# Kernel tuning notes

Measured on AMD Instinct MI355X. Metric: run time of the kernel, lower is better.

## Reference

```python
import jax, jax.numpy as jnp
import numpy as np

L = 6   # n_layers
NH = 8  # num_heads


def _ln(x, g, b, eps=1e-5):
    m = jnp.mean(x, axis=-1, keepdims=True)
    v = jnp.var(x, axis=-1, keepdims=True)
    return (x - m) / jnp.sqrt(v + eps) * g + b


def _mha(q_in, k_in, v_in, Wqkv, bqkv, Wo, bo, bias):
    # Wqkv: [3,H,H], bias: [B,NH,Sq,Sk] or None
    B, Sq, H = q_in.shape
    dk = H // NH
    q = (q_in @ Wqkv[0] + bqkv[0]).reshape(B, Sq, NH, dk).transpose(0, 2, 1, 3)
    k = (k_in @ Wqkv[1] + bqkv[1]).reshape(B, -1, NH, dk).transpose(0, 2, 1, 3)
    v = (v_in @ Wqkv[2] + bqkv[2]).reshape(B, -1, NH, dk).transpose(0, 2, 1, 3)
    scores = jnp.einsum('bhqd,bhkd->bhqk', q * (dk ** -0.5), k)
    if bias is not None:
        scores = scores + bias
    a = jax.nn.softmax(scores, axis=-1)
    o = jnp.einsum('bhqk,bhkd->bhqd', a, v).transpose(0, 2, 1, 3).reshape(B, Sq, H)
    return o @ Wo + bo


def setup_inputs() -> dict:
    key = jax.random.key(0)
    B, N, Din, H, Bd, F, C, G, Dout = 8, 512, 128, 512, 8, 2048, 128, 1, 10
    ks = jax.random.split(key, 20)
    s = 0.02 / np.sqrt(L)
    inp = {
        'x': jax.random.normal(ks[0], (B, N, Din), jnp.float32),
        'attn_bias': jax.random.normal(ks[1], (B, N, N, Bd), jnp.float32),
        'node_W': jax.random.normal(ks[2], (Din, H), jnp.float32) * s,
        'node_b': jnp.zeros((H,), jnp.float32),
        'graph_token': jax.random.normal(ks[3], (G, H), jnp.float32) * 0.02,
        'graph_vd': jax.random.normal(ks[4], (G, Bd), jnp.float32) * 0.02,
        'centroids': jax.random.uniform(ks[5], (C, H), jnp.float32),
        'ln1_g': jnp.ones((L, H), jnp.float32),
        'ln1_b': jnp.zeros((L, H), jnp.float32),
        'Wqkv_loc': jax.random.normal(ks[6], (L, 3, H, H), jnp.float32) * s,
        'bqkv_loc': jnp.zeros((L, 3, H), jnp.float32),
        'Wbias': jax.random.normal(ks[7], (L, Bd, NH), jnp.float32) * s,
        'bbias': jnp.zeros((L, NH), jnp.float32),
        'Wo_loc': jax.random.normal(ks[8], (L, H, H), jnp.float32) * s,
        'bo_loc': jnp.zeros((L, H), jnp.float32),
        'Wqkv_glb': jax.random.normal(ks[9], (L, 3, H, H), jnp.float32) * s,
        'bqkv_glb': jnp.zeros((L, 3, H), jnp.float32),
        'Wo_glb': jax.random.normal(ks[10], (L, H, H), jnp.float32) * s,
        'bo_glb': jnp.zeros((L, H), jnp.float32),
        'ffn_ln_g': jnp.ones((L, 2 * H), jnp.float32),
        'ffn_ln_b': jnp.zeros((L, 2 * H), jnp.float32),
        'W1': jax.random.normal(ks[11], (L, 2 * H, F), jnp.float32) * s,
        'b1': jnp.zeros((L, F), jnp.float32),
        'W2': jax.random.normal(ks[12], (L, F, H), jnp.float32) * s,
        'b2': jnp.zeros((L, H), jnp.float32),
        'final_g': jnp.ones((H,), jnp.float32),
        'final_b': jnp.zeros((H,), jnp.float32),
        'out_W': jax.random.normal(ks[13], (H, Dout), jnp.float32) * s,
        'out_b': jnp.zeros((Dout,), jnp.float32),
    }
    return inp


def reference(x, attn_bias, node_W, node_b, graph_token, graph_vd, centroids,
              ln1_g, ln1_b, Wqkv_loc, bqkv_loc, Wbias, bbias, Wo_loc, bo_loc,
              Wqkv_glb, bqkv_glb, Wo_glb, bo_glb, ffn_ln_g, ffn_ln_b,
              W1, b1, W2, b2, final_g, final_b, out_W, out_b):
    B, N, _ = x.shape
    G = graph_token.shape[0]
    S = N + G
    # node encoder + global node tokens
    h = x @ node_W + node_b                                   # [B,N,H]
    h = jnp.concatenate([h, jnp.broadcast_to(graph_token[None], (B, G, graph_token.shape[1]))], axis=1)  # [B,S,H]
    # extend attn_bias with virtual-distance rows/cols -> [B,S,S,Bd]
    Bd = attn_bias.shape[-1]
    row = jnp.broadcast_to(graph_vd[None, :, None, :], (B, G, N, Bd))
    ab = jnp.concatenate([attn_bias, row], axis=1)            # [B,S,N,Bd]
    col = jnp.broadcast_to(graph_vd[None, None, :, :], (B, S, G, Bd))
    ab = jnp.concatenate([ab, col], axis=2)                   # [B,S,S,Bd]
    # centroids broadcast over batch
    c = jnp.broadcast_to(centroids[None], (B,) + centroids.shape)
    out = h
    for l in range(L):
        bias_l = jnp.einsum('bqkd,dh->bhqk', ab, Wbias[l]) + bbias[l][None, :, None, None]
        y = _ln(out, ln1_g[l], ln1_b[l])
        y = _mha(y, y, y, Wqkv_loc[l], bqkv_loc[l], Wo_loc[l], bo_loc[l], bias_l)
        xr = out + y
        g = _mha(y, c, c, Wqkv_glb[l], bqkv_glb[l], Wo_glb[l], bo_glb[l], None)
        g = xr + g
        y2 = _ln(jnp.concatenate([xr, g], axis=-1), ffn_ln_g[l], ffn_ln_b[l])
        y2 = jax.nn.gelu(y2 @ W1[l] + b1[l], approximate=False) @ W2[l] + b2[l]
        out = xr + y2
    out = _ln(out, final_g, final_b)
    logits = out[:, 0, :] @ out_W + out_b
    return jax.nn.log_softmax(logits, axis=1)
```

## Files before the change

kernel.cpp:

```cpp
#include <hip/hip_runtime.h>
#include <math.h>

typedef unsigned short ushort_t;
typedef __attribute__((ext_vector_type(8))) __bf16 bf16x8;
typedef __attribute__((ext_vector_type(4))) float f32x4;

#define BB 8
#define NN 512
#define HH 512
#define NH 8
#define DKK 64
#define FF 2048
#define CC 128
#define LL 6
#define SS 513
#define SQP 528
#define SPL 544
#define MV 4104
#define MP 4224

__device__ inline float b2f(ushort_t u){ unsigned int x = ((unsigned int)u) << 16; return __uint_as_float(x); }
__device__ inline ushort_t f2b(float f){
    unsigned int x = __float_as_uint(f);
    unsigned int r = (x + 0x7fffu + ((x >> 16) & 1u)) >> 16;
    return (ushort_t)r;
}

__global__ __launch_bounds__(256)
void transpose_cvt_k(const float* __restrict__ in, ushort_t* __restrict__ out, int K, int N){
    __shared__ float t[32][33];
    int z = blockIdx.z;
    in  += (size_t)z * K * N;
    out += (size_t)z * K * N;
    int n0 = blockIdx.x * 32, k0 = blockIdx.y * 32;
    int tx = threadIdx.x, ty = threadIdx.y;
    #pragma unroll
    for (int i = 0; i < 4; i++)
        t[ty + i*8][tx] = in[(size_t)(k0 + ty + i*8) * N + n0 + tx];
    __syncthreads();
    #pragma unroll
    for (int i = 0; i < 4; i++)
        out[(size_t)(n0 + ty + i*8) * K + k0 + tx] = f2b(t[tx][ty + i*8]);
}

__global__ __launch_bounds__(256)
void cvt_k(const float* __restrict__ in, ushort_t* __restrict__ out, int n4){
    int i = blockIdx.x * 256 + threadIdx.x;
    if (i < n4){
        float4 v = ((const float4*)in)[i];
        ushort4 o; o.x = f2b(v.x); o.y = f2b(v.y); o.z = f2b(v.z); o.w = f2b(v.w);
        ((ushort4*)out)[i] = o;
    }
}

__global__ void fill_graph_k(const float* __restrict__ gt, float* __restrict__ resid){
    int b = blockIdx.x, t = threadIdx.x;
    resid[((size_t)(b*SS) + NN)*HH + t] = gt[t];
}

struct EpiP {
    const float* bias;
    float* f0; const float* fin;
    ushort_t* b0; ushort_t* b1; ushort_t* b2;
    int Mvalid;
    int zsB, zsBias, zs0, zs1;
};

template<int EPI>
__global__ __launch_bounds__(256, 2)
void gemm_k(const ushort_t* __restrict__ Abuf, int lda,
            const ushort_t* __restrict__ Bt, int ldb,
            int K, EpiP p)
{
    __shared__ ushort_t As[2][128*64];
    __shared__ ushort_t Bs[2][128*64];
    int tid = threadIdx.x, lane = tid & 63, wave = tid >> 6;
    int z = blockIdx.z;
    Bt += (size_t)z * p.zsB;
    int tm = blockIdx.y * 128, tn = blockIdx.x * 128;
    int r0 = (wave >> 1) * 64, c0 = (wave & 1) * 64;
    int lrow = lane & 15, lk = (lane >> 4) * 8;
    const ushort_t* Ag0 = Abuf + (size_t)tm * lda;
    const ushort_t* Bg0 = Bt   + (size_t)tn * ldb;

    auto stage = [&](int buf, int k0){
        #pragma unroll
        for (int i = 0; i < 4; i++){
            int boff = (i*256 + tid) * 16;
            int row  = boff >> 7;
            int src  = boff ^ ((row & 7) << 4);
            int cole = (src & 127) >> 1;
            __builtin_amdgcn_global_load_lds(
                (const __attribute__((address_space(1))) void*)(Ag0 + (size_t)row*lda + k0 + cole),
                (__attribute__((address_space(3))) void*)((char*)As[buf] + boff), 16, 0, 0);
            __builtin_amdgcn_global_load_lds(
                (const __attribute__((address_space(1))) void*)(Bg0 + (size_t)row*ldb + k0 + cole),
                (__attribute__((address_space(3))) void*)((char*)Bs[buf] + boff), 16, 0, 0);
        }
    };

    f32x4 acc[4][4] = {};
    stage(0, 0);
    int nk = K >> 6;
    for (int kt = 0; kt < nk; kt++){
        int cur = kt & 1;
        __syncthreads();
        if (kt + 1 < nk) stage(cur ^ 1, (kt + 1) * 64);
        const char* Ac = (const char*)As[cur];
        const char* Bc = (const char*)Bs[cur];
        #pragma unroll
        for (int kk = 0; kk < 64; kk += 32){
            bf16x8 af[4], bfv[4];
            #pragma unroll
            for (int i = 0; i < 4; i++){
                int r = r0 + i*16 + lrow;
                int byte = (r*64 + kk + lk)*2;
                byte ^= (r & 7) << 4;
                af[i] = *(const bf16x8*)(Ac + byte);
            }
            #pragma unroll
            for (int j = 0; j < 4; j++){
                int r = c0 + j*16 + lrow;
                int byte = (r*64 + kk + lk)*2;
                byte ^= (r & 7) << 4;
                bfv[j] = *(const bf16x8*)(Bc + byte);
            }
            #pragma unroll
            for (int i = 0; i < 4; i++)
                #pragma unroll
                for (int j = 0; j < 4; j++)
                    acc[i][j] = __builtin_amdgcn_mfma_f32_16x16x32_bf16(af[i], bfv[j], acc[i][j], 0, 0, 0);
        }
    }
    const float* biasp = p.bias ? (p.bias + (size_t)z * p.zsBias) : nullptr;
    #pragma unroll
    for (int i = 0; i < 4; i++)
    #pragma unroll
    for (int j = 0; j < 4; j++)
    #pragma unroll
    for (int r = 0; r < 4; r++){
        int grow = tm + r0 + i*16 + (lane >> 4)*4 + r;
        int gcol = tn + c0 + j*16 + (lane & 15);
        if (grow >= p.Mvalid) continue;
        float v = acc[i][j][r] + (biasp ? biasp[gcol] : 0.f);
        if constexpr (EPI == 0){
            int rg = (grow >> 9) * SS + (grow & 511);
            p.f0[(size_t)rg * HH + gcol] = v;
        } else if constexpr (EPI == 1){
            int b = grow / SS, s = grow - b * SS;
            int mat = gcol >> 9, c = gcol & 511, h = c >> 6, d = c & 63;
            if (mat == 0)      p.b0[(((size_t)(b*NH + h))*SQP + s)*DKK + d] = f2b(v);
            else if (mat == 1) p.b1[(((size_t)(b*NH + h))*SPL + s)*DKK + d] = f2b(v);
            else               p.b2[(((size_t)(b*NH + h))*DKK + d)*SPL + s] = f2b(v);
        } else if constexpr (EPI == 2){
            int mat = gcol >> 9, c = gcol & 511, h = c >> 6, d = c & 63;
            if (mat == 0) (p.b0 + (size_t)z*p.zs0)[((size_t)h*CC + grow)*DKK + d] = f2b(v);
            else          (p.b1 + (size_t)z*p.zs1)[((size_t)h*DKK + d)*CC + grow] = f2b(v);
        } else if constexpr (EPI == 3){
            int b = grow / SS, s = grow - b * SS, h = gcol >> 6, d = gcol & 63;
            p.b0[(((size_t)(b*NH + h))*SQP + s)*DKK + d] = f2b(v);
        } else if constexpr (EPI == 4){
            p.b0[(size_t)grow*HH + gcol] = f2b(v);
            p.f0[(size_t)grow*HH + gcol] = p.fin[(size_t)grow*HH + gcol] + v;
        } else if constexpr (EPI == 5){
            p.f0[(size_t)grow*HH + gcol] = p.fin[(size_t)grow*HH + gcol] + v;
        } else if constexpr (EPI == 6){
            float t = 0.5f * v * (1.f + erff(v * 0.70710678118f));
            p.b0[(size_t)grow*FF + gcol] = f2b(t);
        } else if constexpr (EPI == 7){
            p.f0[(size_t)grow*HH + gcol] = p.fin[(size_t)grow*HH + gcol] + v;
        }
    }
}

__global__ __launch_bounds__(128)
void ln512_k(const float* __restrict__ in, const float* __restrict__ g,
             const float* __restrict__ bb, ushort_t* __restrict__ out){
    int row = blockIdx.x, t = threadIdx.x;
    float4 v = ((const float4*)(in + (size_t)row*HH))[t];
    float s  = v.x + v.y + v.z + v.w;
    float s2 = v.x*v.x + v.y*v.y + v.z*v.z + v.w*v.w;
    #pragma unroll
    for (int o = 1; o < 64; o <<= 1){ s += __shfl_xor(s, o); s2 += __shfl_xor(s2, o); }
    __shared__ float ps[2], ps2[2];
    if ((t & 63) == 0){ ps[t >> 6] = s; ps2[t >> 6] = s2; }
    __syncthreads();
    s = ps[0] + ps[1]; s2 = ps2[0] + ps2[1];
    float mean = s * (1.f/512.f);
    float var  = s2 * (1.f/512.f) - mean*mean;
    float rstd = rsqrtf(var + 1e-5f);
    float4 gv = ((const float4*)g)[t];
    float4 bv = ((const float4*)bb)[t];
    ushort4 o4;
    o4.x = f2b((v.x - mean)*rstd*gv.x + bv.x);
    o4.y = f2b((v.y - mean)*rstd*gv.y + bv.y);
    o4.z = f2b((v.z - mean)*rstd*gv.z + bv.z);
    o4.w = f2b((v.w - mean)*rstd*gv.w + bv.w);
    ((ushort4*)(out + (size_t)row*HH))[t] = o4;
}

__global__ __launch_bounds__(128)
void ln1024_k(const float* __restrict__ xr, const float* __restrict__ gb,
              const float* __restrict__ g, const float* __restrict__ bb,
              ushort_t* __restrict__ out){
    int row = blockIdx.x, t = threadIdx.x;
    const float* src = (t < 64) ? (xr + (size_t)row*HH + t*8) : (gb + (size_t)row*HH + (t-64)*8);
    float4 v0 = ((const float4*)src)[0];
    float4 v1 = ((const float4*)src)[1];
    float s  = v0.x+v0.y+v0.z+v0.w + v1.x+v1.y+v1.z+v1.w;
    float s2 = v0.x*v0.x+v0.y*v0.y+v0.z*v0.z+v0.w*v0.w + v1.x*v1.x+v1.y*v1.y+v1.z*v1.z+v1.w*v1.w;
    #pragma unroll
    for (int o = 1; o < 64; o <<= 1){ s += __shfl_xor(s, o); s2 += __shfl_xor(s2, o); }
    __shared__ float ps[2], ps2[2];
    if ((t & 63) == 0){ ps[t >> 6] = s; ps2[t >> 6] = s2; }
    __syncthreads();
    s = ps[0] + ps[1]; s2 = ps2[0] + ps2[1];
    float mean = s * (1.f/1024.f);
    float var  = s2 * (1.f/1024.f) - mean*mean;
    float rstd = rsqrtf(var + 1e-5f);
    int col = (t < 64) ? t*8 : 512 + (t-64)*8;
    float vv[8] = {v0.x,v0.y,v0.z,v0.w,v1.x,v1.y,v1.z,v1.w};
    ushort4 oa, ob;
    float r0 = (vv[0]-mean)*rstd*g[col+0] + bb[col+0];
    float r1 = (vv[1]-mean)*rstd*g[col+1] + bb[col+1];
    float r2 = (vv[2]-mean)*rstd*g[col+2] + bb[col+2];
    float r3 = (vv[3]-mean)*rstd*g[col+3] + bb[col+3];
    float r4 = (vv[4]-mean)*rstd*g[col+4] + bb[col+4];
    float r5 = (vv[5]-mean)*rstd*g[col+5] + bb[col+5];
    float r6 = (vv[6]-mean)*rstd*g[col+6] + bb[col+6];
    float r7 = (vv[7]-mean)*rstd*g[col+7] + bb[col+7];
    oa.x=f2b(r0); oa.y=f2b(r1); oa.z=f2b(r2); oa.w=f2b(r3);
    ob.x=f2b(r4); ob.y=f2b(r5); ob.z=f2b(r6); ob.w=f2b(r7);
    ushort_t* op = out + (size_t)row*1024 + col;
    ((ushort4*)op)[0] = oa; ((ushort4*)op)[1] = ob;
}

__global__ __launch_bounds__(128)
void bias_k(const float* __restrict__ ab, const float* __restrict__ gvd,
            const float* __restrict__ Wb, const float* __restrict__ bbv,
            ushort_t* __restrict__ outp){
    __shared__ float w[64];
    __shared__ float bb[8];
    int t = threadIdx.x;
    if (t < 64) w[t] = Wb[t];
    if (t < 8)  bb[t] = bbv[t];
    __syncthreads();
    int kk = blockIdx.x * 128 + t;
    if (kk >= SS) return;
    int q = blockIdx.y, b = blockIdx.z;
    float a[8];
    if (q < NN && kk < NN){
        const float4* p = (const float4*)(ab + ((((size_t)b*NN + q)*NN) + kk)*8);
        float4 x = p[0], y = p[1];
        a[0]=x.x; a[1]=x.y; a[2]=x.z; a[3]=x.w; a[4]=y.x; a[5]=y.y; a[6]=y.z; a[7]=y.w;
    } else {
        #pragma unroll
        for (int d = 0; d < 8; d++) a[d] = gvd[d];
    }
    #pragma unroll
    for (int h = 0; h < 8; h++){
        float val = bb[h];
        #pragma unroll
        for (int d = 0; d < 8; d++) val += a[d] * w[d*8 + h];
        outp[(((size_t)(b*NH + h)*SS + q)*SS) + kk] = f2b(val);
    }
}

__global__ __launch_bounds__(128)
void bias_all_k(const float* __restrict__ ab, const float* __restrict__ gvd,
                const float* __restrict__ Wb , const float* __restrict__ bbv ,
                ushort_t* __restrict__ outp){
    __shared__ float w[LL*64];
    __shared__ float bb[LL*8];
    int t = threadIdx.x;
    for (int i = t; i < LL*64; i += 128) w[i] = Wb[i];
    for (int i = t; i < LL*8;  i += 128) bb[i] = bbv[i];
    __syncthreads();
    int kk = blockIdx.x * 128 + t;
    if (kk >= SS) return;
    int q = blockIdx.y, b = blockIdx.z;
    float a[8];
    if (q < NN && kk < NN){
        const float4* p = (const float4*)(ab + ((((size_t)b*NN + q)*NN) + kk)*8);
        float4 x = p[0], y = p[1];
        a[0]=x.x; a[1]=x.y; a[2]=x.z; a[3]=x.w; a[4]=y.x; a[5]=y.y; a[6]=y.z; a[7]=y.w;
    } else {
        #pragma unroll
        for (int d = 0; d < 8; d++) a[d] = gvd[d];
    }
    #pragma unroll
    for (int l = 0; l < LL; l++){
        #pragma unroll
        for (int h = 0; h < 8; h++){
            float val = bb[l*8 + h];
            #pragma unroll
            for (int d = 0; d < 8; d++) val += a[d] * w[l*64 + d*8 + h];
            outp[((((size_t)l*BB + b)*NH + h)*SS + q)*SS + kk] = f2b(val);
        }
    }
}

__global__ __launch_bounds__(256)
void attn_k(const ushort_t* __restrict__ q, const ushort_t* __restrict__ kbuf,
            const ushort_t* __restrict__ vt, const ushort_t* __restrict__ bias,
            ushort_t* __restrict__ outp,
            int Skv, int nsteps, int kRows, int vCols, int kvBstrK, int kvBstrV, float scale){
    __shared__ float ptile[4][16*36];
    __shared__ float combO[4][16][64];
    __shared__ float combL[4][16];

    int qt = blockIdx.x, h = blockIdx.y, b = blockIdx.z;
    int tid = threadIdx.x, lane = tid & 63, w = tid >> 6;
    int lrow = lane & 15, seg = lane >> 4;
    int q0 = qt * 16;
    const ushort_t* qb = q    + ((size_t)(b*NH + h))*SQP*DKK;
    const ushort_t* kb = kbuf + (size_t)b*kvBstrK + (size_t)h*kRows*DKK;
    const ushort_t* vb = vt   + (size_t)b*kvBstrV + (size_t)h*DKK*vCols;
    const ushort_t* bb = bias ? (bias + ((size_t)(b*NH + h))*SS*SS) : nullptr;

    bf16x8 qf0 = *(const bf16x8*)(qb + (size_t)(q0 + lrow)*DKK + seg*8);
    bf16x8 qf1 = *(const bf16x8*)(qb + (size_t)(q0 + lrow)*DKK + 32 + seg*8);

    float l_[4] = {0.f, 0.f, 0.f, 0.f};
    f32x4 O[4] = {};
    float* pt = &ptile[w][0];

    for (int t = w; t < nsteps; t += 4){
        int pos0 = t * 32;
        f32x4 sA = {0.f,0.f,0.f,0.f}, sB = {0.f,0.f,0.f,0.f};
        if (pos0 < Skv){
            bf16x8 kf0 = *(const bf16x8*)(kb + (size_t)(pos0 + lrow)*DKK + seg*8);
            bf16x8 kf1 = *(const bf16x8*)(kb + (size_t)(pos0 + lrow)*DKK + 32 + seg*8);
            sA = __builtin_amdgcn_mfma_f32_16x16x32_bf16(qf0, kf0, sA, 0, 0, 0);
            sA = __builtin_amdgcn_mfma_f32_16x16x32_bf16(qf1, kf1, sA, 0, 0, 0);
        }
        if (pos0 + 16 < Skv){
            bf16x8 kf0 = *(const bf16x8*)(kb + (size_t)(pos0 + 16 + lrow)*DKK + seg*8);
            bf16x8 kf1 = *(const bf16x8*)(kb + (size_t)(pos0 + 16 + lrow)*DKK + 32 + seg*8);
            sB = __builtin_amdgcn_mfma_f32_16x16x32_bf16(qf0, kf0, sB, 0, 0, 0);
            sB = __builtin_amdgcn_mfma_f32_16x16x32_bf16(qf1, kf1, sB, 0, 0, 0);
        }
        float pa[4], pb[4];
        if (pos0 + 32 <= Skv){
            #pragma unroll
            for (int r = 0; r < 4; r++){
                int qq = q0 + seg*4 + r; if (qq >= SS) qq = SS - 1;
                float sa = sA[r] * scale, sb = sB[r] * scale;
                if (bb){
                    sa += b2f(bb[(size_t)qq*SS + pos0 + lrow]);
                    sb += b2f(bb[(size_t)qq*SS + pos0 + 16 + lrow]);
                }
                pa[r] = __expf(sa); pb[r] = __expf(sb);
            }
        } else {
            int colA = pos0 + lrow, colB = pos0 + 16 + lrow;
            #pragma unroll
            for (int r = 0; r < 4; r++){
                int qq = q0 + seg*4 + r; if (qq >= SS) qq = SS - 1;
                float sa = sA[r] * scale, sb = sB[r] * scale;
                if (bb){
                    if (colA < Skv) sa += b2f(bb[(size_t)qq*SS + colA]);
                    if (colB < Skv) sb += b2f(bb[(size_t)qq*SS + colB]);
                }
                pa[r] = (colA < Skv) ? __expf(sa) : 0.f;
                pb[r] = (colB < Skv) ? __expf(sb) : 0.f;
            }
        }
        #pragma unroll
        for (int r = 0; r < 4; r++){
            l_[r] += pa[r] + pb[r];
            pt[(seg*4 + r)*36 + lrow]      = pa[r];
            pt[(seg*4 + r)*36 + 16 + lrow] = pb[r];
        }
        asm volatile("s_waitcnt lgkmcnt(0)" ::: "memory");
        f32x4 pA = *(const f32x4*)&pt[lrow*36 + seg*8];
        f32x4 pB = *(const f32x4*)&pt[lrow*36 + seg*8 + 4];
        unsigned int u0, u1, u2, u3;
        asm volatile("v_cvt_pk_bf16_f32 %0, %1, %2" : "=v"(u0) : "v"(pA[0]), "v"(pA[1]));
        asm volatile("v_cvt_pk_bf16_f32 %0, %1, %2" : "=v"(u1) : "v"(pA[2]), "v"(pA[3]));
        asm volatile("v_cvt_pk_bf16_f32 %0, %1, %2" : "=v"(u2) : "v"(pB[0]), "v"(pB[1]));
        asm volatile("v_cvt_pk_bf16_f32 %0, %1, %2" : "=v"(u3) : "v"(pB[2]), "v"(pB[3]));
        bf16x8 pf;
        ((unsigned int*)&pf)[0] = u0; ((unsigned int*)&pf)[1] = u1;
        ((unsigned int*)&pf)[2] = u2; ((unsigned int*)&pf)[3] = u3;
        #pragma unroll
        for (int j = 0; j < 4; j++){
            bf16x8 vf = *(const bf16x8*)(vb + (size_t)(j*16 + lrow)*vCols + pos0 + seg*8);
            O[j] = __builtin_amdgcn_mfma_f32_16x16x32_bf16(pf, vf, O[j], 0, 0, 0);
        }
    }
    #pragma unroll
    for (int r = 0; r < 4; r++){
        float v = l_[r];
        v += __shfl_xor(v, 1); v += __shfl_xor(v, 2);
        v += __shfl_xor(v, 4); v += __shfl_xor(v, 8);
        if (lrow == 0) combL[w][seg*4 + r] = v;
    }
    #pragma unroll
    for (int j = 0; j < 4; j++)
        #pragma unroll
        for (int r = 0; r < 4; r++)
            combO[w][seg*4 + r][j*16 + lrow] = O[j][r];
    __syncthreads();
    int qrow = tid >> 4, d0 = (tid & 15) * 4;
    float Lt = combL[0][qrow] + combL[1][qrow] + combL[2][qrow] + combL[3][qrow];
    f32x4 a = {0.f,0.f,0.f,0.f};
    #pragma unroll
    for (int ww = 0; ww < 4; ww++){
        f32x4 o = *(const f32x4*)&combO[ww][qrow][d0];
        a[0] += o[0]; a[1] += o[1]; a[2] += o[2]; a[3] += o[3];
    }
    float inv = 1.f / Lt;
    int qq = q0 + qrow;
    if (qq < SS){
        ushort4 o4; o4.x = f2b(a[0]*inv); o4.y = f2b(a[1]*inv); o4.z = f2b(a[2]*inv); o4.w = f2b(a[3]*inv);
        *(ushort4*)(outp + ((size_t)(b*SS + qq))*HH + h*DKK + d0) = o4;
    }
}

__global__ __launch_bounds__(64)
void final_k(const float* __restrict__ resid, const float* __restrict__ fg,
             const float* __restrict__ fb, const float* __restrict__ outW,
             const float* __restrict__ outb, float* __restrict__ outp){
    int b = blockIdx.x, lane = threadIdx.x;
    const float* r = resid + (size_t)b*SS*HH;
    float4 v0 = ((const float4*)r)[lane*2];
    float4 v1 = ((const float4*)r)[lane*2 + 1];
    float vv[8] = {v0.x,v0.y,v0.z,v0.w,v1.x,v1.y,v1.z,v1.w};
    float s = 0.f, s2 = 0.f;
    #pragma unroll
    for (int i = 0; i < 8; i++){ s += vv[i]; s2 += vv[i]*vv[i]; }
    #pragma unroll
    for (int o = 1; o < 64; o <<= 1){ s += __shfl_xor(s, o); s2 += __shfl_xor(s2, o); }
    float mean = s * (1.f/512.f);
    float var  = s2 * (1.f/512.f) - mean*mean;
    float rstd = rsqrtf(var + 1e-5f);
    int base = lane * 8;
    float n[8];
    #pragma unroll
    for (int i = 0; i < 8; i++) n[i] = (vv[i]-mean)*rstd*fg[base+i] + fb[base+i];
    float lg[10];
    #pragma unroll
    for (int j = 0; j < 10; j++){
        float p = 0.f;
        #pragma unroll
        for (int i = 0; i < 8; i++) p += n[i] * outW[(size_t)(base+i)*10 + j];
        #pragma unroll
        for (int o = 1; o < 64; o <<= 1) p += __shfl_xor(p, o);
        lg[j] = p;
    }
    if (lane == 0){
        float m = -1e30f;
        #pragma unroll
        for (int j = 0; j < 10; j++){ lg[j] += outb[j]; m = fmaxf(m, lg[j]); }
        float se = 0.f;
        #pragma unroll
        for (int j = 0; j < 10; j++) se += __expf(lg[j] - m);
        float ls = m + logf(se);
        #pragma unroll
        for (int j = 0; j < 10; j++) outp[b*10 + j] = lg[j] - ls;
    }
}

extern "C" void kernel_launch(void* const* d_in, const int* in_sizes, int n_in,
                              void* d_out, int out_size, void* d_ws, size_t ws_size,
                              hipStream_t stream){
    const float* x         = (const float*)d_in[0];
    const float* attn_bias = (const float*)d_in[1];
    const float* node_W    = (const float*)d_in[2];
    const float* node_b    = (const float*)d_in[3];
    const float* graph_tok = (const float*)d_in[4];
    const float* graph_vd  = (const float*)d_in[5];
    const float* centroids = (const float*)d_in[6];
    const float* ln1_g     = (const float*)d_in[7];
    const float* ln1_b     = (const float*)d_in[8];
    const float* Wqkv_loc  = (const float*)d_in[9];
    const float* bqkv_loc  = (const float*)d_in[10];
    const float* Wbias     = (const float*)d_in[11];
    const float* bbias     = (const float*)d_in[12];
    const float* Wo_loc    = (const float*)d_in[13];
    const float* bo_loc    = (const float*)d_in[14];
    const float* Wqkv_glb  = (const float*)d_in[15];
    const float* bqkv_glb  = (const float*)d_in[16];
    const float* Wo_glb    = (const float*)d_in[17];
    const float* bo_glb    = (const float*)d_in[18];
    const float* ffn_ln_g  = (const float*)d_in[19];
    const float* ffn_ln_b  = (const float*)d_in[20];
    const float* W1        = (const float*)d_in[21];
    const float* b1        = (const float*)d_in[22];
    const float* W2        = (const float*)d_in[23];
    const float* b2        = (const float*)d_in[24];
    const float* final_g   = (const float*)d_in[25];
    const float* final_b   = (const float*)d_in[26];
    const float* out_W     = (const float*)d_in[27];
    const float* out_b     = (const float*)d_in[28];

    char* base = (char*)d_ws; size_t off = 0;
    auto alloc = [&](size_t n) -> void* { void* p = base + off; off = (off + n + 255) & ~(size_t)255; return p; };
    float*    resid = (float*)alloc((size_t)MP*HH*4);
    float*    xr    = (float*)alloc((size_t)MP*HH*4);
    float*    gbuf  = (float*)alloc((size_t)MP*HH*4);
    ushort_t* ybf   = (ushort_t*)alloc((size_t)MP*HH*2);
    ushort_t* ymha  = (ushort_t*)alloc((size_t)MP*HH*2);
    ushort_t* aout  = (ushort_t*)alloc((size_t)MP*HH*2);
    ushort_t* qb    = (ushort_t*)alloc((size_t)BB*NH*SQP*DKK*2);
    ushort_t* kb    = (ushort_t*)alloc((size_t)BB*NH*SPL*DKK*2);
    ushort_t* vtb   = (ushort_t*)alloc((size_t)BB*NH*DKK*SPL*2);
    ushort_t* kc6   = (ushort_t*)alloc((size_t)LL*NH*CC*DKK*2);
    ushort_t* vc6   = (ushort_t*)alloc((size_t)LL*NH*DKK*CC*2);
    ushort_t* cat   = (ushort_t*)alloc((size_t)MP*1024*2);
    ushort_t* mid   = (ushort_t*)alloc((size_t)MP*FF*2);
    ushort_t* xbf   = (ushort_t*)alloc((size_t)4096*128*2);
    ushort_t* cbf   = (ushort_t*)alloc((size_t)CC*HH*2);
    ushort_t* nodeWt= (ushort_t*)alloc((size_t)HH*128*2);
    ushort_t* WqkvLt= (ushort_t*)alloc((size_t)LL*3*HH*HH*2);
    ushort_t* WoLt  = (ushort_t*)alloc((size_t)LL*HH*HH*2);
    ushort_t* WqkvGt= (ushort_t*)alloc((size_t)LL*3*HH*HH*2);
    ushort_t* WoGt  = (ushort_t*)alloc((size_t)LL*HH*HH*2);
    ushort_t* W1t   = (ushort_t*)alloc((size_t)LL*FF*1024*2);
    ushort_t* W2t   = (ushort_t*)alloc((size_t)LL*HH*FF*2);
    size_t planeSz = (size_t)BB*NH*SS*SS;
    bool mode6 = (ws_size > off + (size_t)LL*planeSz*2 + 4096);
    ushort_t* biasL = (ushort_t*)alloc((mode6 ? (size_t)LL : 1) * planeSz * 2);
    (void)in_sizes; (void)n_in; (void)out_size;

    dim3 tb(32, 8);
    transpose_cvt_k<<<dim3(HH/32, 128/32, 1),  tb, 0, stream>>>(node_W,   nodeWt, 128,  HH);
    transpose_cvt_k<<<dim3(HH/32, HH/32, 18),  tb, 0, stream>>>(Wqkv_loc, WqkvLt, HH,   HH);
    transpose_cvt_k<<<dim3(HH/32, HH/32, 6),   tb, 0, stream>>>(Wo_loc,   WoLt,   HH,   HH);
    transpose_cvt_k<<<dim3(HH/32, HH/32, 18),  tb, 0, stream>>>(Wqkv_glb, WqkvGt, HH,   HH);
    transpose_cvt_k<<<dim3(HH/32, HH/32, 6),   tb, 0, stream>>>(Wo_glb,   WoGt,   HH,   HH);
    transpose_cvt_k<<<dim3(FF/32, 1024/32, 6), tb, 0, stream>>>(W1,       W1t,    1024, FF);
    transpose_cvt_k<<<dim3(HH/32, FF/32, 6),   tb, 0, stream>>>(W2,       W2t,    FF,   HH);
    cvt_k<<<512, 256, 0, stream>>>(x, xbf, 4096*128/4);
    cvt_k<<<64,  256, 0, stream>>>(centroids, cbf, CC*HH/4);

    {
        EpiP p{}; p.bias = node_b; p.f0 = resid; p.Mvalid = 4096;
        gemm_k<0><<<dim3(HH/128, 4096/128), 256, 0, stream>>>(xbf, 128, nodeWt, 128, 128, p);
    }
    fill_graph_k<<<BB, HH, 0, stream>>>(graph_tok, resid);

    if (mode6)
        bias_all_k<<<dim3(5, SS, BB), 128, 0, stream>>>(attn_bias, graph_vd, Wbias, bbias, biasL);

    {
        EpiP p{}; p.bias = bqkv_glb + HH; p.zsBias = 3*HH;
        p.b0 = kc6; p.zs0 = NH*CC*DKK; p.b1 = vc6; p.zs1 = NH*DKK*CC;
        p.zsB = 3*HH*HH; p.Mvalid = CC;
        gemm_k<2><<<dim3(1024/128, 1, LL), 256, 0, stream>>>(cbf, HH,
                WqkvGt + (size_t)HH*HH, HH, HH, p);
    }

    for (int l = 0; l < LL; l++){
        ushort_t* biasCur = biasL + (mode6 ? (size_t)l*planeSz : 0);
        if (!mode6)
            bias_k<<<dim3(5, SS, BB), 128, 0, stream>>>(attn_bias, graph_vd,
                    Wbias + l*64, bbias + l*8, biasCur);
        ln512_k<<<MV, 128, 0, stream>>>(resid, ln1_g + l*HH, ln1_b + l*HH, ybf);
        {
            EpiP p{}; p.bias = bqkv_loc + l*3*HH; p.b0 = qb; p.b1 = kb; p.b2 = vtb; p.Mvalid = MV;
            gemm_k<1><<<dim3(1536/128, MP/128), 256, 0, stream>>>(ybf, HH,
                    WqkvLt + (size_t)l*3*HH*HH, HH, HH, p);
        }
        attn_k<<<dim3(33, NH, BB), 256, 0, stream>>>(qb, kb, vtb, biasCur, aout,
                SS, 17, SPL, SPL, NH*SPL*DKK, NH*DKK*SPL, 0.125f);
        {
            EpiP p{}; p.bias = bo_loc + l*HH; p.b0 = ymha; p.f0 = xr; p.fin = resid; p.Mvalid = MV;
            gemm_k<4><<<dim3(HH/128, MP/128), 256, 0, stream>>>(aout, HH,
                    WoLt + (size_t)l*HH*HH, HH, HH, p);
        }
        {
            EpiP p{}; p.bias = bqkv_glb + l*3*HH; p.b0 = qb; p.Mvalid = MV;
            gemm_k<3><<<dim3(HH/128, MP/128), 256, 0, stream>>>(ymha, HH,
                    WqkvGt + (size_t)l*3*HH*HH, HH, HH, p);
        }
        attn_k<<<dim3(33, NH, BB), 256, 0, stream>>>(qb, kc6 + (size_t)l*NH*CC*DKK,
                vc6 + (size_t)l*NH*DKK*CC, nullptr, aout,
                CC, 4, CC, CC, 0, 0, 0.125f);
        {
            EpiP p{}; p.bias = bo_glb + l*HH; p.f0 = gbuf; p.fin = xr; p.Mvalid = MV;
            gemm_k<5><<<dim3(HH/128, MP/128), 256, 0, stream>>>(aout, HH,
                    WoGt + (size_t)l*HH*HH, HH, HH, p);
        }
        ln1024_k<<<MV, 128, 0, stream>>>(xr, gbuf, ffn_ln_g + l*1024, ffn_ln_b + l*1024, cat);
        {
            EpiP p{}; p.bias = b1 + l*FF; p.b0 = mid; p.Mvalid = MV;
            gemm_k<6><<<dim3(FF/128, MP/128), 256, 0, stream>>>(cat, 1024,
                    W1t + (size_t)l*FF*1024, 1024, 1024, p);
        }
        {
            EpiP p{}; p.bias = b2 + l*HH; p.f0 = resid; p.fin = xr; p.Mvalid = MV;
            gemm_k<7><<<dim3(HH/128, MP/128), 256, 0, stream>>>(mid, FF,
                    W2t + (size_t)l*HH*FF, FF, FF, p);
        }
    }
    final_k<<<BB, 64, 0, stream>>>(resid, final_g, final_b, out_W, out_b, (float*)d_out);
}
```

Measured before the change: 2.182 ms.

## Shrink GEMM tiles to 64-row blocks and drop LDS double buffering

Templates the GEMM kernel on wave count, so blocks become 64 rows by 64 or 128 columns with one or two waves, replacing the 128x128 four-wave tile. It also removes LDS double buffering: each k-step loads and then syncs before compute, with a second barrier after. The smaller tiles raise block count and occupancy for the N=512 GEMMs on a many-CU GPU. In exchange, operands get less reuse, more global traffic goes to A and B reloads, and load latency is no longer hidden behind MFMA work.

```diff
diff --git a/kernel.cpp b/kernel.cpp
--- a/kernel.cpp
+++ b/kernel.cpp
@@ -66,54 +66,58 @@
     int zsB, zsBias, zs0, zs1;
 };
 
-template<int EPI>
-__global__ __launch_bounds__(256, 2)
+template<int EPI, int NW>
+__global__ __launch_bounds__(NW*64, 2)
 void gemm_k(const ushort_t* __restrict__ Abuf, int lda,
             const ushort_t* __restrict__ Bt, int ldb,
             int K, EpiP p)
 {
-    __shared__ ushort_t As[2][128*64];
-    __shared__ ushort_t Bs[2][128*64];
+    __shared__ ushort_t As[64*64];
+    __shared__ ushort_t Bs[NW*64*64];
+    constexpr int NT = NW * 64;
+    constexpr int LA = 8 / NW;
     int tid = threadIdx.x, lane = tid & 63, wave = tid >> 6;
     int z = blockIdx.z;
     Bt += (size_t)z * p.zsB;
-    int tm = blockIdx.y * 128, tn = blockIdx.x * 128;
-    int r0 = (wave >> 1) * 64, c0 = (wave & 1) * 64;
+    int tm = blockIdx.y * 64, tn = blockIdx.x * NT;
+    int c0 = wave * 64;
     int lrow = lane & 15, lk = (lane >> 4) * 8;
     const ushort_t* Ag0 = Abuf + (size_t)tm * lda;
     const ushort_t* Bg0 = Bt   + (size_t)tn * ldb;
 
-    auto stage = [&](int buf, int k0){
-        #pragma unroll
-        for (int i = 0; i < 4; i++){
-            int boff = (i*256 + tid) * 16;
+    f32x4 acc[4][4] = {};
+    int nk = K >> 6;
+    for (int kt = 0; kt < nk; kt++){
+        int k0 = kt * 64;
+        #pragma unroll
+        for (int i = 0; i < LA; i++){
+            int boff = (i*NT + tid) * 16;
             int row  = boff >> 7;
             int src  = boff ^ ((row & 7) << 4);
             int cole = (src & 127) >> 1;
             __builtin_amdgcn_global_load_lds(
                 (const __attribute__((address_space(1))) void*)(Ag0 + (size_t)row*lda + k0 + cole),
-                (__attribute__((address_space(3))) void*)((char*)As[buf] + boff), 16, 0, 0);
+                (__attribute__((address_space(3))) void*)((char*)As + boff), 16, 0, 0);
+        }
+        #pragma unroll
+        for (int i = 0; i < 8; i++){
+            int boff = (i*NT + tid) * 16;
+            int row  = boff >> 7;
+            int src  = boff ^ ((row & 7) << 4);
+            int cole = (src & 127) >> 1;
             __builtin_amdgcn_global_load_lds(
                 (const __attribute__((address_space(1))) void*)(Bg0 + (size_t)row*ldb + k0 + cole),
-                (__attribute__((address_space(3))) void*)((char*)Bs[buf] + boff), 16, 0, 0);
-        }
-    };
-
-    f32x4 acc[4][4] = {};
-    stage(0, 0);
-    int nk = K >> 6;
-    for (int kt = 0; kt < nk; kt++){
-        int cur = kt & 1;
+                (__attribute__((address_space(3))) void*)((char*)Bs + boff), 16, 0, 0);
+        }
         __syncthreads();
-        if (kt + 1 < nk) stage(cur ^ 1, (kt + 1) * 64);
-        const char* Ac = (const char*)As[cur];
-        const char* Bc = (const char*)Bs[cur];
+        const char* Ac = (const char*)As;
+        const char* Bc = (const char*)Bs;
         #pragma unroll
         for (int kk = 0; kk < 64; kk += 32){
             bf16x8 af[4], bfv[4];
             #pragma unroll
             for (int i = 0; i < 4; i++){
-                int r = r0 + i*16 + lrow;
+                int r = i*16 + lrow;
                 int byte = (r*64 + kk + lk)*2;
                 byte ^= (r & 7) << 4;
                 af[i] = *(const bf16x8*)(Ac + byte);
@@ -131,6 +135,7 @@
                 for (int j = 0; j < 4; j++)
                     acc[i][j] = __builtin_amdgcn_mfma_f32_16x16x32_bf16(af[i], bfv[j], acc[i][j], 0, 0, 0);
         }
+        __syncthreads();
     }
     const float* biasp = p.bias ? (p.bias + (size_t)z * p.zsBias) : nullptr;
     #pragma unroll
@@ -139,7 +144,7 @@
     for (int j = 0; j < 4; j++)
     #pragma unroll
     for (int r = 0; r < 4; r++){
-        int grow = tm + r0 + i*16 + (lane >> 4)*4 + r;
+        int grow = tm + i*16 + (lane >> 4)*4 + r;
         int gcol = tn + c0 + j*16 + (lane & 15);
         if (grow >= p.Mvalid) continue;
         float v = acc[i][j][r] + (biasp ? biasp[gcol] : 0.f);
@@ -537,7 +542,7 @@
 
     {
         EpiP p{}; p.bias = node_b; p.f0 = resid; p.Mvalid = 4096;
-        gemm_k<0><<<dim3(HH/128, 4096/128), 256, 0, stream>>>(xbf, 128, nodeWt, 128, 128, p);
+        gemm_k<0,2><<<dim3(HH/128, 4096/64), 128, 0, stream>>>(xbf, 128, nodeWt, 128, 128, p);
     }
     fill_graph_k<<<BB, HH, 0, stream>>>(graph_tok, resid);
 
@@ -548,7 +553,7 @@
         EpiP p{}; p.bias = bqkv_glb + HH; p.zsBias = 3*HH;
         p.b0 = kc6; p.zs0 = NH*CC*DKK; p.b1 = vc6; p.zs1 = NH*DKK*CC;
         p.zsB = 3*HH*HH; p.Mvalid = CC;
-        gemm_k<2><<<dim3(1024/128, 1, LL), 256, 0, stream>>>(cbf, HH,
+        gemm_k<2,2><<<dim3(1024/128, CC/64, LL), 128, 0, stream>>>(cbf, HH,
                 WqkvGt + (size_t)HH*HH, HH, HH, p);
     }
 
@@ -560,19 +565,19 @@
         ln512_k<<<MV, 128, 0, stream>>>(resid, ln1_g + l*HH, ln1_b + l*HH, ybf);
         {
             EpiP p{}; p.bias = bqkv_loc + l*3*HH; p.b0 = qb; p.b1 = kb; p.b2 = vtb; p.Mvalid = MV;
-            gemm_k<1><<<dim3(1536/128, MP/128), 256, 0, stream>>>(ybf, HH,
+            gemm_k<1,2><<<dim3(1536/128, MP/64), 128, 0, stream>>>(ybf, HH,
                     WqkvLt + (size_t)l*3*HH*HH, HH, HH, p);
         }
         attn_k<<<dim3(33, NH, BB), 256, 0, stream>>>(qb, kb, vtb, biasCur, aout,
                 SS, 17, SPL, SPL, NH*SPL*DKK, NH*DKK*SPL, 0.125f);
         {
             EpiP p{}; p.bias = bo_loc + l*HH; p.b0 = ymha; p.f0 = xr; p.fin = resid; p.Mvalid = MV;
-            gemm_k<4><<<dim3(HH/128, MP/128), 256, 0, stream>>>(aout, HH,
+            gemm_k<4,1><<<dim3(HH/64, MP/64), 64, 0, stream>>>(aout, HH,
                     WoLt + (size_t)l*HH*HH, HH, HH, p);
         }
         {
             EpiP p{}; p.bias = bqkv_glb + l*3*HH; p.b0 = qb; p.Mvalid = MV;
-            gemm_k<3><<<dim3(HH/128, MP/128), 256, 0, stream>>>(ymha, HH,
+            gemm_k<3,1><<<dim3(HH/64, MP/64), 64, 0, stream>>>(ymha, HH,
                     WqkvGt + (size_t)l*3*HH*HH, HH, HH, p);
         }
         attn_k<<<dim3(33, NH, BB), 256, 0, stream>>>(qb, kc6 + (size_t)l*NH*CC*DKK,
@@ -580,18 +585,18 @@
                 CC, 4, CC, CC, 0, 0, 0.125f);
         {
             EpiP p{}; p.bias = bo_glb + l*HH; p.f0 = gbuf; p.fin = xr; p.Mvalid = MV;
-            gemm_k<5><<<dim3(HH/128, MP/128), 256, 0, stream>>>(aout, HH,
+            gemm_k<5,1><<<dim3(HH/64, MP/64), 64, 0, stream>>>(aout, HH,
                     WoGt + (size_t)l*HH*HH, HH, HH, p);
         }
         ln1024_k<<<MV, 128, 0, stream>>>(xr, gbuf, ffn_ln_g + l*1024, ffn_ln_b + l*1024, cat);
         {
             EpiP p{}; p.bias = b1 + l*FF; p.b0 = mid; p.Mvalid = MV;
-            gemm_k<6><<<dim3(FF/128, MP/128), 256, 0, stream>>>(cat, 1024,
+            gemm_k<6,2><<<dim3(FF/128, MP/64), 128, 0, stream>>>(cat, 1024,
                     W1t + (size_t)l*FF*1024, 1024, 1024, p);
         }
         {
             EpiP p{}; p.bias = b2 + l*HH; p.f0 = resid; p.fin = xr; p.Mvalid = MV;
-            gemm_k<7><<<dim3(HH/128, MP/128), 256, 0, stream>>>(mid, FF,
+            gemm_k<7,1><<<dim3(HH/64, MP/64), 64, 0, stream>>>(mid, FF,
                     W2t + (size_t)l*HH*FF, FF, FF, p);
         }
     }
```

Result: faster. 2.047 ms (-6.2%).
